# Optimization experiments

Hardware: AMD Instinct MI355X
Metric: run time of the kernel (lower is better)

The kernel has to match this reference:

```python
import jax, jax.numpy as jnp
import numpy as np

P, F, FR = 288, 7, 12      # time slots per day, days per week, sampling frequency scale
CHEB_K = 2
HID = 64


def _ste(time_index, SE, W_se, b_se, T_tod, T_dow):
    """Spatio-temporal embedding: learned spatial embedding projected to et_dim,
    plus time-of-day and day-of-week temporal embeddings. -> [B, N, et]"""
    t = time_index * FR
    tod = T_tod[t % P]                 # [B, et]
    dow = T_dow[(t // P) % F]          # [B, et]
    se = SE @ W_se + b_se              # [N, et]
    return se[None, :, :] + (tod + dow)[:, None, :]


def _avwgcn(x, STE, R, SC, Wpool, bpool):
    """Adaptive-vertex-weight graph conv (AGCRN-style) with dynamic STE-driven
    adjacency blended with dynamic relation R and static correlation SC.
    x: [B,N,Cin], STE: [B,N,et], R: [B,N,N], SC: [N,N]."""
    A = jax.nn.softmax(
        jax.nn.relu(jnp.einsum('bnd,bmd->bnm', STE, STE)) + R + SC[None], axis=-1)
    # Chebyshev polynomial supports applied to x (T0 = I handled implicitly)
    xs = [x, jnp.einsum('bnm,bmc->bnc', A, x)]
    for _ in range(CHEB_K - 2):
        xs.append(2.0 * jnp.einsum('bnm,bmc->bnc', A, xs[-1]) - xs[-2])
    x_g = jnp.stack(xs, axis=2)                        # [B,N,K,Cin]
    # per-node adaptive weights: W_n = STE @ Wpool; contracted without
    # materializing the [B,N,K,Cin,Cout] tensor
    g = jnp.einsum('bnki,dkio->bndo', x_g, Wpool)      # [B,N,et,Cout]
    out = jnp.einsum('bndo,bnd->bno', g, STE) + jnp.einsum('bnd,do->bno', STE, bpool)
    return out


def setup_inputs() -> dict:
    key = jax.random.key(0)
    ks = jax.random.split(key, 12)
    B, N, Din, et, es = 32, 1024, 1, 16, 16
    std = 0.1
    return {
        "x": jax.random.normal(ks[0], (B, N, Din), jnp.float32),
        "R": jax.random.normal(ks[1], (B, N, N), jnp.float32) * std,
        "state": jax.random.normal(ks[2], (B, N, HID), jnp.float32),
        "SC": jax.random.normal(ks[3], (N, N), jnp.float32) * std,
        "SE": jax.random.normal(ks[4], (N, es), jnp.float32),
        "W_se": jax.random.normal(ks[5], (es, et), jnp.float32) * std,
        "b_se": jnp.zeros((et,), jnp.float32),
        "T_tod": jax.random.normal(ks[6], (P, et), jnp.float32) * std,
        "T_dow": jax.random.normal(ks[7], (F, et), jnp.float32) * std,
        "W_gate": jax.random.normal(ks[8], (et, CHEB_K, Din + HID, 2 * HID), jnp.float32) * std,
        "b_gate": jnp.zeros((et, 2 * HID), jnp.float32),
        "W_upd": jax.random.normal(ks[9], (et, CHEB_K, Din + HID, HID), jnp.float32) * std,
        "b_upd": jnp.zeros((et, HID), jnp.float32),
        "time_index": jax.random.randint(ks[10], (B,), 0, P * F),
    }


def reference(x, R, state, SC, SE, W_se, b_se, T_tod, T_dow,
              W_gate, b_gate, W_upd, b_upd, time_index):
    STE = _ste(time_index, SE, W_se, b_se, T_tod, T_dow)       # [B,N,et]
    ins = jnp.concatenate([x, state], axis=-1)                 # [B,N,Din+H]
    z_r = jax.nn.sigmoid(_avwgcn(ins, STE, R, SC, W_gate, b_gate))
    z, r = jnp.split(z_r, 2, axis=-1)                          # each [B,N,H]
    cand = jnp.concatenate([x, z * state], axis=-1)
    hc = jnp.tanh(_avwgcn(cand, STE, R, SC, W_upd, b_upd))
    return r * state + (1.0 - r) * hc                          # [B,N,H]
```

## Files before the change

kernel.cpp:

```cpp
#include <hip/hip_runtime.h>
#include <math.h>

namespace {
constexpr int BB = 32;
constexpr int NN = 1024;
constexpr int ET = 16;
constexpr int HH = 64;
constexpr int CIN = 65;
constexpr int KI = 2*CIN;
constexpr int COG = 2*HH;
constexpr int COU = HH;
constexpr int PP = 288;
constexpr int FF = 7;
constexpr int FRQ = 12;
constexpr int XK = 160;

typedef __attribute__((ext_vector_type(4))) float f32x4;
typedef __attribute__((ext_vector_type(8))) short s16x8;
typedef unsigned long long ull;

__device__ __forceinline__ float bf2f(unsigned short u) {
    unsigned v = ((unsigned)u) << 16;
    return __builtin_bit_cast(float, v);
}
__device__ __forceinline__ unsigned short f2bf(float f) {
    unsigned u = __builtin_bit_cast(unsigned, f);
    u += 0x7fffu + ((u >> 16) & 1u);
    return (unsigned short)(u >> 16);
}
__device__ __forceinline__ unsigned cvtpk(float lo, float hi) {
    unsigned r;
    asm("v_cvt_pk_bf16_f32 %0, %1, %2" : "=v"(r) : "v"(lo), "v"(hi));
    return r;
}
__device__ __forceinline__ float ldany(const float* p) { return *p; }
__device__ __forceinline__ float ldany(const unsigned short* p) { return bf2f(*p); }

__global__ void k_prep1(const float* __restrict__ SE, const float* __restrict__ Wse,
                        const float* __restrict__ bse, const float* __restrict__ Ttod,
                        const float* __restrict__ Tdow, const int* __restrict__ tidx,
                        float* __restrict__ se, float* __restrict__ tt) {
    int idx = blockIdx.x*blockDim.x + threadIdx.x;
    if (idx < NN*ET) {
        int n = idx / ET, d = idx % ET;
        float acc = bse[d];
        #pragma unroll
        for (int e = 0; e < ET; ++e) acc += SE[n*ET + e]*Wse[e*ET + d];
        se[idx] = acc;
    } else if (idx < NN*ET + BB*ET) {
        int r = idx - NN*ET;
        int b = r / ET, d = r % ET;
        int t = tidx[b]*FRQ;
        tt[r] = Ttod[(t % PP)*ET + d] + Tdow[((t/PP) % FF)*ET + d];
    }
}

__global__ void k_prep2(const float* __restrict__ se, const float* __restrict__ tt,
                        const float* __restrict__ Wg, const float* __restrict__ Wu,
                        unsigned short* __restrict__ stebf,
                        unsigned short* __restrict__ Wptg, unsigned short* __restrict__ Wptu) {
    int idx = blockIdx.x*blockDim.x + threadIdx.x;
    if (idx < BB*NN*ET) {
        int d = idx % ET;
        int n = (idx/ET) % NN;
        int b = idx/(ET*NN);
        stebf[idx] = f2bf(se[n*ET+d] + tt[b*ET+d]);
        return;
    }
    idx -= BB*NN*ET;
    if (idx < ET*COG*XK) {
        int d = idx/(COG*XK), r = idx%(COG*XK), o = r/XK, ki = r%XK;
        float v = (ki < KI) ? Wg[((size_t)d*KI + ki)*COG + o] : 0.f;
        Wptg[((size_t)d*COG + o)*XK + ki] = f2bf(v);
        return;
    }
    idx -= ET*COG*XK;
    if (idx < ET*COU*XK) {
        int d = idx/(COU*XK), r = idx%(COU*XK), o = r/XK, ki = r%XK;
        float v = (ki < KI) ? Wu[((size_t)d*KI + ki)*COU + o] : 0.f;
        Wptu[((size_t)d*COU + o)*XK + ki] = f2bf(v);
    }
}

template<typename T>
__global__ void k_vin(const float* __restrict__ x, const T* __restrict__ sv,
                      unsigned short* __restrict__ xgbf, unsigned short* __restrict__ vt) {
    int idx = blockIdx.x*blockDim.x + threadIdx.x;
    if (idx < BB*128*64) {
        int och = idx & 63, mb = (idx >> 6) & 127, b = idx >> 13;
        const T* src = sv + ((size_t)b*NN + mb*8)*HH + och;
        float v0=ldany(src), v1=ldany(src+HH), v2=ldany(src+2*HH), v3=ldany(src+3*HH);
        float v4=ldany(src+4*HH), v5=ldany(src+5*HH), v6=ldany(src+6*HH), v7=ldany(src+7*HH);
        ull lo = (ull)f2bf(v0) | ((ull)f2bf(v1)<<16) | ((ull)f2bf(v2)<<32) | ((ull)f2bf(v3)<<48);
        ull hi = (ull)f2bf(v4) | ((ull)f2bf(v5)<<16) | ((ull)f2bf(v6)<<32) | ((ull)f2bf(v7)<<48);
        ull* dst = (ull*)(vt + (size_t)idx*8);
        dst[0] = lo; dst[1] = hi;
        return;
    }
    idx -= BB*128*64;
    if (idx >= BB*NN*(XK/2)) return;
    int row = idx/(XK/2), c = idx%(XK/2);
    if (c < 32) {
        int k0 = 2*c;
        float v0 = (k0 == 0) ? x[row] : ldany(sv + (size_t)row*HH + k0 - 1);
        float v1 = ldany(sv + (size_t)row*HH + k0);
        ((unsigned*)xgbf)[(size_t)row*(XK/2) + c] = ((unsigned)f2bf(v1) << 16) | f2bf(v0);
    } else if (c == 32) {
        xgbf[(size_t)row*XK + 64] = f2bf(ldany(sv + (size_t)row*HH + 63));
    } else if (c >= 65) {
        ((unsigned*)xgbf)[(size_t)row*(XK/2) + c] = 0;
    }
}

constexpr int SSTR   = 1048;
constexpr int S_OFF  = 0;
constexpr int XV_OFF = 33536;
constexpr int MSH_OFF  = 37632;
constexpr int MSHC_OFF = 37888;
constexpr int LP_OFF   = 37952;
constexpr int AXP_OFF  = 38208;
constexpr int LSH_OFF  = 38464;
constexpr int SMEM_BYTES = 38528;

template<int PASS>
__global__ __launch_bounds__(256, 4) void k_attn(
    const unsigned short* __restrict__ stebf, const float* __restrict__ Rg,
    const float* __restrict__ SCg, const float* __restrict__ xg,
    const unsigned short* __restrict__ vt,
    float* __restrict__ Mr, float* __restrict__ Li,
    unsigned short* __restrict__ xgout, unsigned short* __restrict__ pglob)
{
    extern __shared__ char smem[];
    const int t = threadIdx.x, lane = t & 63, w = t >> 6;
    const int c15 = lane & 15, g = lane >> 4;
    const int strip = blockIdx.x, b = blockIdx.y;
    const size_t bN = (size_t)b * NN;
    const int r0 = strip * 16;

    float* Mshf  = (float*)(smem + MSH_OFF);
    float* MshCf = (float*)(smem + MSHC_OFF);
    float* Lpf   = (float*)(smem + LP_OFF);
    float* Axpf  = (float*)(smem + AXP_OFF);
    float* Lshf  = (float*)(smem + LSH_OFF);

    if (PASS == 1) {
        ((float4*)(smem + XV_OFF))[t] = ((const float4*)(xg + bN))[t];
    } else {
        if (t < 16) Lshf[t] = Li[bN + r0 + t];
    }
    float mp2 = 0.f;
    if (PASS == 2) mp2 = Mr[bN + r0 + c15];

    float mx = -INFINITY;
    {
        s16x8 bfr = {0,0,0,0,0,0,0,0};
        if (g < 2) bfr = *(const s16x8*)(stebf + (bN + r0 + c15)*ET + g*8);
        const float* Rb  = Rg  + (bN + r0 + c15)*NN;
        const float* SCb = SCg + (size_t)(r0 + c15)*NN;
        const int colq = w*16 + g*4;
        s16x8 af0 = {0,0,0,0,0,0,0,0}, af1 = {0,0,0,0,0,0,0,0};
        if (g < 2) {
            af0 = *(const s16x8*)(stebf + (bN + 0*64 + w*16 + c15)*ET + g*8);
            af1 = *(const s16x8*)(stebf + (bN + 1*64 + w*16 + c15)*ET + g*8);
        }
        float4 rc0 = *(const float4*)(Rb + colq);
        float4 sc0 = *(const float4*)(SCb + colq);
        float4 rc1 = *(const float4*)(Rb + colq + 64);
        float4 sc1 = *(const float4*)(SCb + colq + 64);
        #pragma unroll
        for (int j = 0; j < 16; ++j) {
            s16x8 afc = af0; af0 = af1;
            float4 rcc = rc0, scc = sc0;
            rc0 = rc1; sc0 = sc1;
            if (j < 14) {
                if (g < 2) af1 = *(const s16x8*)(stebf + (bN + (j+2)*64 + w*16 + c15)*ET + g*8);
                rc1 = *(const float4*)(Rb + colq + (j+2)*64);
                sc1 = *(const float4*)(SCb + colq + (j+2)*64);
            }
            f32x4 zero = {0.f,0.f,0.f,0.f};
            f32x4 d = __builtin_amdgcn_mfma_f32_16x16x32_bf16(afc, bfr, zero, 0, 0, 0);
            float s0 = fmaxf(d[0],0.f) + rcc.x + scc.x;
            float s1 = fmaxf(d[1],0.f) + rcc.y + scc.y;
            float s2 = fmaxf(d[2],0.f) + rcc.z + scc.z;
            float s3 = fmaxf(d[3],0.f) + rcc.w + scc.w;
            unsigned byteo = (unsigned)(c15*SSTR + j*64 + colq)*2u;
            if (PASS == 1) {
                mx = fmaxf(mx, fmaxf(fmaxf(s0,s1), fmaxf(s2,s3)));
                *(ull*)(smem + S_OFF + byteo) = (ull)cvtpk(s0,s1) | ((ull)cvtpk(s2,s3) << 32);
            } else {
                float p0 = __expf(s0 - mp2), p1 = __expf(s1 - mp2);
                float p2 = __expf(s2 - mp2), p3 = __expf(s3 - mp2);
                *(ull*)(smem + S_OFF + byteo) = (ull)cvtpk(p0,p1) | ((ull)cvtpk(p2,p3) << 32);
            }
        }
    }

    if (PASS == 1) {
        mx = fmaxf(mx, __shfl_xor(mx, 16));
        mx = fmaxf(mx, __shfl_xor(mx, 32));
        if (lane < 16) Mshf[w*16 + c15] = mx;
        __syncthreads();
        if (t < 16) {
            float M = fmaxf(fmaxf(Mshf[t], Mshf[16+t]), fmaxf(Mshf[32+t], Mshf[48+t]));
            MshCf[t] = M;
            Mr[bN + r0 + t] = M;
        }
        __syncthreads();
        const float m = MshCf[c15];
        const int colq = w*16 + g*4;
        float L = 0.f, ax = 0.f;
        for (int it = 0; it < 16; ++it) {
            unsigned byteo = (unsigned)(c15*SSTR + it*64 + colq)*2u;
            ull v = *(ull*)(smem + S_OFF + byteo);
            float s0 = bf2f((unsigned short)v);
            float s1 = bf2f((unsigned short)(v >> 16));
            float s2 = bf2f((unsigned short)(v >> 32));
            float s3 = bf2f((unsigned short)(v >> 48));
            float p0 = __expf(s0-m), p1 = __expf(s1-m), p2 = __expf(s2-m), p3 = __expf(s3-m);
            float4 xq = *(const float4*)(smem + XV_OFF + (it*64 + colq)*4);
            L += (p0 + p1) + (p2 + p3);
            ax += p0*xq.x + p1*xq.y + p2*xq.z + p3*xq.w;
            ull pk = (ull)cvtpk(p0,p1) | ((ull)cvtpk(p2,p3) << 32);
            *(ull*)(smem + S_OFF + byteo) = pk;
            if (pglob) *(ull*)(pglob + (bN + r0 + c15)*1024 + it*64 + colq) = pk;
        }
        L += __shfl_xor(L, 16); L += __shfl_xor(L, 32);
        ax += __shfl_xor(ax, 16); ax += __shfl_xor(ax, 32);
        if (lane < 16) { Lpf[w*16 + c15] = L; Axpf[w*16 + c15] = ax; }
        __syncthreads();
        if (t < 16) {
            float Lt = Lpf[t] + Lpf[16+t] + Lpf[32+t] + Lpf[48+t];
            float li = 1.f / Lt;
            Lshf[t] = li;
            Li[bN + r0 + t] = li;
            float axt = Axpf[t] + Axpf[16+t] + Axpf[32+t] + Axpf[48+t];
            xgout[(bN + r0 + t)*XK + 65] = f2bf(axt * li);
        }
        __syncthreads();
    } else {
        __syncthreads();
    }

    {
        f32x4 acc = {0.f,0.f,0.f,0.f};
        const unsigned short* vtb = vt + (size_t)b*65536 + (w*16 + c15)*8 + g*512;
        s16x8 bv0 = *(const s16x8*)(vtb);
        s16x8 bv1 = *(const s16x8*)(vtb + 2048);
        #pragma unroll
        for (int kk = 0; kk < 32; ++kk) {
            s16x8 bvc = bv0; bv0 = bv1;
            if (kk < 30) bv1 = *(const s16x8*)(vtb + (size_t)(kk+2)*2048);
            s16x8 a = *(const s16x8*)(smem + S_OFF + (unsigned)(c15*SSTR + kk*32 + g*8)*2u);
            acc = __builtin_amdgcn_mfma_f32_16x16x32_bf16(a, bvc, acc, 0, 0, 0);
        }
        #pragma unroll
        for (int q = 0; q < 4; ++q) {
            int rowl = g*4 + q;
            float li = Lshf[rowl];
            xgout[(bN + r0 + rowl)*XK + 66 + w*16 + c15] = f2bf(acc[q] * li);
        }
    }
}

__global__ __launch_bounds__(256) void k_pv2(
    const unsigned short* __restrict__ pglob, const unsigned short* __restrict__ vt,
    const float* __restrict__ Li, unsigned short* __restrict__ xgout)
{
    const int t = threadIdx.x, lane = t & 63, w = t >> 6;
    const int c15 = lane & 15, g = lane >> 4;
    const int b = blockIdx.y;
    const int strip = blockIdx.x*4 + w;
    const size_t bN = (size_t)b*NN;
    const int r0 = strip*16;

    const unsigned short* Pr  = pglob + (bN + r0 + c15)*1024 + g*8;
    const unsigned short* vb0 = vt + (size_t)b*65536 + c15*8 + g*512;

    f32x4 acc0 = {0,0,0,0}, acc1 = {0,0,0,0}, acc2 = {0,0,0,0}, acc3 = {0,0,0,0};
    s16x8 a0 = *(const s16x8*)(Pr);
    s16x8 a1 = *(const s16x8*)(Pr + 32);
    #pragma unroll 8
    for (int kk = 0; kk < 32; ++kk) {
        s16x8 ac = a0; a0 = a1;
        if (kk < 30) a1 = *(const s16x8*)(Pr + (kk+2)*32);
        const unsigned short* vb = vb0 + (size_t)kk*2048;
        s16x8 b0 = *(const s16x8*)(vb);
        s16x8 b1 = *(const s16x8*)(vb + 128);
        s16x8 b2 = *(const s16x8*)(vb + 256);
        s16x8 b3 = *(const s16x8*)(vb + 384);
        acc0 = __builtin_amdgcn_mfma_f32_16x16x32_bf16(ac, b0, acc0, 0, 0, 0);
        acc1 = __builtin_amdgcn_mfma_f32_16x16x32_bf16(ac, b1, acc1, 0, 0, 0);
        acc2 = __builtin_amdgcn_mfma_f32_16x16x32_bf16(ac, b2, acc2, 0, 0, 0);
        acc3 = __builtin_amdgcn_mfma_f32_16x16x32_bf16(ac, b3, acc3, 0, 0, 0);
    }
    #pragma unroll
    for (int q = 0; q < 4; ++q) {
        int row = r0 + g*4 + q;
        float li = Li[bN + row];
        unsigned short* op = xgout + (bN + row)*XK + 66 + c15;
        op[0]  = f2bf(acc0[q]*li);
        op[16] = f2bf(acc1[q]*li);
        op[32] = f2bf(acc2[q]*li);
        op[48] = f2bf(acc3[q]*li);
    }
}

template<int COUT, int EPI>
__global__ __launch_bounds__(256, 2) void k_apply(
    const unsigned short* __restrict__ Wpt, const float* __restrict__ bias,
    const unsigned short* __restrict__ stebf, const unsigned short* __restrict__ xgbf,
    const float* __restrict__ state, unsigned short* __restrict__ zsbf,
    unsigned short* __restrict__ rrbf, float* __restrict__ out)
{
    const int t = threadIdx.x, lane = t & 63, w = t >> 6;
    const int c15 = lane & 15, g = lane >> 4;
    const int n0 = blockIdx.x*32, b = blockIdx.y, oh = blockIdx.z;
    const int o = oh*64 + w*16 + c15;

    f32x4 acc[16][2];
    #pragma unroll
    for (int d = 0; d < 16; ++d) {
        acc[d][0] = (f32x4){0.f,0.f,0.f,0.f};
        acc[d][1] = (f32x4){0.f,0.f,0.f,0.f};
    }

    const unsigned short* Ar0 = xgbf + ((size_t)b*NN + n0 + c15)*XK + g*8;
    const unsigned short* Ar1 = Ar0 + (size_t)16*XK;
    const unsigned short* Bp  = Wpt + (size_t)o*XK + g*8;

    for (int ks = 0; ks < 5; ++ks) {
        s16x8 a0 = *(const s16x8*)(Ar0 + ks*32);
        s16x8 a1 = *(const s16x8*)(Ar1 + ks*32);
        #pragma unroll
        for (int d = 0; d < 16; ++d) {
            s16x8 bf = *(const s16x8*)(Bp + (size_t)d*COUT*XK + ks*32);
            acc[d][0] = __builtin_amdgcn_mfma_f32_16x16x32_bf16(a0, bf, acc[d][0], 0, 0, 0);
            acc[d][1] = __builtin_amdgcn_mfma_f32_16x16x32_bf16(a1, bf, acc[d][1], 0, 0, 0);
        }
    }

    float biasv[16];
    #pragma unroll
    for (int d = 0; d < 16; ++d) biasv[d] = bias[d*COUT + o];

    #pragma unroll
    for (int mt = 0; mt < 2; ++mt) {
        #pragma unroll
        for (int q = 0; q < 4; ++q) {
            int n = n0 + mt*16 + g*4 + q;
            size_t bn = (size_t)b*NN + n;
            const ull* sp = (const ull*)(stebf + bn*ET);
            float val = 0.f;
            #pragma unroll
            for (int dd = 0; dd < 4; ++dd) {
                ull sv4 = sp[dd];
                float s0 = bf2f((unsigned short)sv4);
                float s1 = bf2f((unsigned short)(sv4 >> 16));
                float s2 = bf2f((unsigned short)(sv4 >> 32));
                float s3 = bf2f((unsigned short)(sv4 >> 48));
                val += s0*(acc[dd*4+0][mt][q] + biasv[dd*4+0]);
                val += s1*(acc[dd*4+1][mt][q] + biasv[dd*4+1]);
                val += s2*(acc[dd*4+2][mt][q] + biasv[dd*4+2]);
                val += s3*(acc[dd*4+3][mt][q] + biasv[dd*4+3]);
            }
            if (EPI == 0) {
                float gv = 1.f/(1.f + __expf(-val));
                if (oh == 0) zsbf[bn*HH + o] = f2bf(gv * state[bn*HH + o]);
                else         rrbf[bn*HH + (o - 64)] = f2bf(gv);
            } else {
                float hc = tanhf(val);
                float rv = bf2f(rrbf[bn*HH + o]);
                out[bn*HH + o] = rv*state[bn*HH + o] + (1.f - rv)*hc;
            }
        }
    }
}

}

extern "C" void kernel_launch(void* const* d_in, const int* in_sizes, int n_in,
                              void* d_out, int out_size, void* d_ws, size_t ws_size,
                              hipStream_t stream) {
    const float* x     = (const float*)d_in[0];
    const float* R     = (const float*)d_in[1];
    const float* state = (const float*)d_in[2];
    const float* SC    = (const float*)d_in[3];
    const float* SE    = (const float*)d_in[4];
    const float* W_se  = (const float*)d_in[5];
    const float* b_se  = (const float*)d_in[6];
    const float* T_tod = (const float*)d_in[7];
    const float* T_dow = (const float*)d_in[8];
    const float* W_g   = (const float*)d_in[9];
    const float* b_g   = (const float*)d_in[10];
    const float* W_u   = (const float*)d_in[11];
    const float* b_u   = (const float*)d_in[12];
    const int*   tidx  = (const int*)d_in[13];
    float* out = (float*)d_out;
    float* ws = (float*)d_ws;

    float* se = ws;
    float* tt = se + 16384;
    float* Mr = tt + 512;
    float* Li = Mr + 32768;
    unsigned short* stebf = (unsigned short*)(Li + 32768);
    unsigned short* xgbf  = stebf + 524288;
    unsigned short* zsbf  = xgbf + 5242880;
    unsigned short* rrbf  = zsbf + 2097152;
    unsigned short* vt    = rrbf + 2097152;
    unsigned short* Wptg  = vt + 2097152;
    unsigned short* Wptu  = Wptg + 327680;
    unsigned short* pglob = Wptu + 163840;
    size_t need_bytes = (size_t)((char*)(pglob + 33554432) - (char*)ws);
    const bool haveP = ws_size >= need_bytes;

    k_prep1<<<66, 256, 0, stream>>>(SE, W_se, b_se, T_tod, T_dow, tidx, se, tt);
    k_prep2<<<3968, 256, 0, stream>>>(se, tt, W_g, W_u, stebf, Wptg, Wptu);

    k_vin<float><<<11264, 256, 0, stream>>>(x, state, xgbf, vt);
    k_attn<1><<<dim3(64, 32), 256, SMEM_BYTES, stream>>>(
        stebf, R, SC, x, vt, Mr, Li, xgbf, haveP ? pglob : nullptr);
    k_apply<COG, 0><<<dim3(32, 32, 2), 256, 0, stream>>>(
        Wptg, b_g, stebf, xgbf, state, zsbf, rrbf, nullptr);

    k_vin<unsigned short><<<11264, 256, 0, stream>>>(x, zsbf, xgbf, vt);
    if (haveP) {
        k_pv2<<<dim3(16, 32), 256, 0, stream>>>(pglob, vt, Li, xgbf);
    } else {
        k_attn<2><<<dim3(64, 32), 256, SMEM_BYTES, stream>>>(
            stebf, R, SC, x, vt, Mr, Li, xgbf, nullptr);
    }
    k_apply<COU, 1><<<dim3(32, 32, 1), 256, 0, stream>>>(
        Wptu, b_u, stebf, xgbf, state, zsbf, rrbf, out);
}
```

Measured before the change: 256.1 us.

## Store P in MFMA-fragment layout and split PV2 per strip across waves

The pass-1 softmax normalization now has each thread handle 8 contiguous columns of one row. Row sums are reduced with intra-16-lane shuffles instead of a shared-memory cross-wave reduction plus an extra barrier. The global probability matrix is written in a strip-major, MFMA-fragment-ordered layout, so the second-pass PV kernel can fetch A operands with fully coalesced 16-byte loads. k_pv2 is restructured to one strip per block, with each wave computing a 16-column output slice, and launches 4x more blocks to raise parallelism. The cost is that each P tile is now reloaded by four waves instead of being shared across four accumulators.

```diff
diff --git a/kernel.cpp b/kernel.cpp
--- a/kernel.cpp
+++ b/kernel.cpp
@@ -17,6 +17,7 @@
 
 typedef __attribute__((ext_vector_type(4))) float f32x4;
 typedef __attribute__((ext_vector_type(8))) short s16x8;
+typedef __attribute__((ext_vector_type(4))) unsigned int u32x4;
 typedef unsigned long long ull;
 
 __device__ __forceinline__ float bf2f(unsigned short u) {
@@ -139,8 +140,6 @@
 
     float* Mshf  = (float*)(smem + MSH_OFF);
     float* MshCf = (float*)(smem + MSHC_OFF);
-    float* Lpf   = (float*)(smem + LP_OFF);
-    float* Axpf  = (float*)(smem + AXP_OFF);
     float* Lshf  = (float*)(smem + LSH_OFF);
 
     if (PASS == 1) {
@@ -206,35 +205,43 @@
             Mr[bN + r0 + t] = M;
         }
         __syncthreads();
-        const float m = MshCf[c15];
-        const int colq = w*16 + g*4;
+        const int rowS = t >> 4, colblk = t & 15;
+        const float m = MshCf[rowS];
+        const size_t stripbase = ((size_t)b*64 + strip)*16384;
         float L = 0.f, ax = 0.f;
-        for (int it = 0; it < 16; ++it) {
-            unsigned byteo = (unsigned)(c15*SSTR + it*64 + colq)*2u;
-            ull v = *(ull*)(smem + S_OFF + byteo);
-            float s0 = bf2f((unsigned short)v);
-            float s1 = bf2f((unsigned short)(v >> 16));
-            float s2 = bf2f((unsigned short)(v >> 32));
-            float s3 = bf2f((unsigned short)(v >> 48));
-            float p0 = __expf(s0-m), p1 = __expf(s1-m), p2 = __expf(s2-m), p3 = __expf(s3-m);
-            float4 xq = *(const float4*)(smem + XV_OFF + (it*64 + colq)*4);
-            L += (p0 + p1) + (p2 + p3);
-            ax += p0*xq.x + p1*xq.y + p2*xq.z + p3*xq.w;
-            ull pk = (ull)cvtpk(p0,p1) | ((ull)cvtpk(p2,p3) << 32);
-            *(ull*)(smem + S_OFF + byteo) = pk;
-            if (pglob) *(ull*)(pglob + (bN + r0 + c15)*1024 + it*64 + colq) = pk;
-        }
-        L += __shfl_xor(L, 16); L += __shfl_xor(L, 32);
-        ax += __shfl_xor(ax, 16); ax += __shfl_xor(ax, 32);
-        if (lane < 16) { Lpf[w*16 + c15] = L; Axpf[w*16 + c15] = ax; }
-        __syncthreads();
-        if (t < 16) {
-            float Lt = Lpf[t] + Lpf[16+t] + Lpf[32+t] + Lpf[48+t];
-            float li = 1.f / Lt;
-            Lshf[t] = li;
-            Li[bN + r0 + t] = li;
-            float axt = Axpf[t] + Axpf[16+t] + Axpf[32+t] + Axpf[48+t];
-            xgout[(bN + r0 + t)*XK + 65] = f2bf(axt * li);
+        #pragma unroll
+        for (int i = 0; i < 8; ++i) {
+            unsigned byteo = (unsigned)(rowS*SSTR + colblk*8 + i*128)*2u;
+            s16x8 sv = *(const s16x8*)(smem + S_OFF + byteo);
+            float p0 = __expf(bf2f((unsigned short)sv[0]) - m);
+            float p1 = __expf(bf2f((unsigned short)sv[1]) - m);
+            float p2 = __expf(bf2f((unsigned short)sv[2]) - m);
+            float p3 = __expf(bf2f((unsigned short)sv[3]) - m);
+            float p4 = __expf(bf2f((unsigned short)sv[4]) - m);
+            float p5 = __expf(bf2f((unsigned short)sv[5]) - m);
+            float p6 = __expf(bf2f((unsigned short)sv[6]) - m);
+            float p7 = __expf(bf2f((unsigned short)sv[7]) - m);
+            float4 xq0 = *(const float4*)(smem + XV_OFF + (unsigned)(colblk*8 + i*128)*4u);
+            float4 xq1 = *(const float4*)(smem + XV_OFF + (unsigned)(colblk*8 + i*128 + 4)*4u);
+            L += ((p0+p1)+(p2+p3)) + ((p4+p5)+(p6+p7));
+            ax += p0*xq0.x + p1*xq0.y + p2*xq0.z + p3*xq0.w
+                + p4*xq1.x + p5*xq1.y + p6*xq1.z + p7*xq1.w;
+            u32x4 pw = { cvtpk(p0,p1), cvtpk(p2,p3), cvtpk(p4,p5), cvtpk(p6,p7) };
+            *(u32x4*)(smem + S_OFF + byteo) = pw;
+            if (pglob) {
+                int cp = colblk + 16*i;
+                *(u32x4*)(pglob + stripbase + (size_t)cp*128 + rowS*8) = pw;
+            }
+        }
+        L += __shfl_xor(L, 1);  ax += __shfl_xor(ax, 1);
+        L += __shfl_xor(L, 2);  ax += __shfl_xor(ax, 2);
+        L += __shfl_xor(L, 4);  ax += __shfl_xor(ax, 4);
+        L += __shfl_xor(L, 8);  ax += __shfl_xor(ax, 8);
+        if ((lane & 15) == 0) {
+            float li = 1.f / L;
+            Lshf[rowS] = li;
+            Li[bN + r0 + rowS] = li;
+            xgout[(bN + r0 + rowS)*XK + 65] = f2bf(ax * li);
         }
         __syncthreads();
     } else {
@@ -262,46 +269,39 @@
     }
 }
 
-__global__ __launch_bounds__(256) void k_pv2(
+__global__ __launch_bounds__(256, 4) void k_pv2(
     const unsigned short* __restrict__ pglob, const unsigned short* __restrict__ vt,
     const float* __restrict__ Li, unsigned short* __restrict__ xgout)
 {
     const int t = threadIdx.x, lane = t & 63, w = t >> 6;
     const int c15 = lane & 15, g = lane >> 4;
-    const int b = blockIdx.y;
-    const int strip = blockIdx.x*4 + w;
+    const int strip = blockIdx.x, b = blockIdx.y;
     const size_t bN = (size_t)b*NN;
     const int r0 = strip*16;
 
-    const unsigned short* Pr  = pglob + (bN + r0 + c15)*1024 + g*8;
-    const unsigned short* vb0 = vt + (size_t)b*65536 + c15*8 + g*512;
-
-    f32x4 acc0 = {0,0,0,0}, acc1 = {0,0,0,0}, acc2 = {0,0,0,0}, acc3 = {0,0,0,0};
-    s16x8 a0 = *(const s16x8*)(Pr);
-    s16x8 a1 = *(const s16x8*)(Pr + 32);
-    #pragma unroll 8
+    const unsigned short* pA = pglob + ((size_t)b*64 + strip)*16384 + (size_t)lane*8;
+    const unsigned short* pB = vt + (size_t)b*65536 + (w*16 + c15)*8 + g*512;
+
+    f32x4 acc = {0.f,0.f,0.f,0.f};
+    s16x8 a0 = *(const s16x8*)(pA);
+    s16x8 b0 = *(const s16x8*)(pB);
+    s16x8 a1 = *(const s16x8*)(pA + 512);
+    s16x8 b1 = *(const s16x8*)(pB + 2048);
+    #pragma unroll
     for (int kk = 0; kk < 32; ++kk) {
-        s16x8 ac = a0; a0 = a1;
-        if (kk < 30) a1 = *(const s16x8*)(Pr + (kk+2)*32);
-        const unsigned short* vb = vb0 + (size_t)kk*2048;
-        s16x8 b0 = *(const s16x8*)(vb);
-        s16x8 b1 = *(const s16x8*)(vb + 128);
-        s16x8 b2 = *(const s16x8*)(vb + 256);
-        s16x8 b3 = *(const s16x8*)(vb + 384);
-        acc0 = __builtin_amdgcn_mfma_f32_16x16x32_bf16(ac, b0, acc0, 0, 0, 0);
-        acc1 = __builtin_amdgcn_mfma_f32_16x16x32_bf16(ac, b1, acc1, 0, 0, 0);
-        acc2 = __builtin_amdgcn_mfma_f32_16x16x32_bf16(ac, b2, acc2, 0, 0, 0);
-        acc3 = __builtin_amdgcn_mfma_f32_16x16x32_bf16(ac, b3, acc3, 0, 0, 0);
+        s16x8 ac = a0, bc = b0;
+        a0 = a1; b0 = b1;
+        if (kk < 30) {
+            a1 = *(const s16x8*)(pA + (size_t)(kk+2)*512);
+            b1 = *(const s16x8*)(pB + (size_t)(kk+2)*2048);
+        }
+        acc = __builtin_amdgcn_mfma_f32_16x16x32_bf16(ac, bc, acc, 0, 0, 0);
     }
     #pragma unroll
     for (int q = 0; q < 4; ++q) {
         int row = r0 + g*4 + q;
         float li = Li[bN + row];
-        unsigned short* op = xgout + (bN + row)*XK + 66 + c15;
-        op[0]  = f2bf(acc0[q]*li);
-        op[16] = f2bf(acc1[q]*li);
-        op[32] = f2bf(acc2[q]*li);
-        op[48] = f2bf(acc3[q]*li);
+        xgout[(bN + row)*XK + 66 + w*16 + c15] = f2bf(acc[q]*li);
     }
 }
 
@@ -424,7 +424,7 @@
 
     k_vin<unsigned short><<<11264, 256, 0, stream>>>(x, zsbf, xgbf, vt);
     if (haveP) {
-        k_pv2<<<dim3(16, 32), 256, 0, stream>>>(pglob, vt, Li, xgbf);
+        k_pv2<<<dim3(64, 32), 256, 0, stream>>>(pglob, vt, Li, xgbf);
     } else {
         k_attn<2><<<dim3(64, 32), 256, SMEM_BYTES, stream>>>(
             stebf, R, SC, x, vt, Mr, Li, xgbf, nullptr);
```

Result: faster. 251.0 us (-2.0%).
